# Kernel optimization log

Measured on AMD Instinct MI355X. Metric: run time of the kernel, lower is better.

## Reference

```python
import jax, jax.numpy as jnp
import numpy as np

H = 2048          # hidden_size
NH = 16           # num attention heads
NKV = 4           # num kv heads (GQA)
HD = 128          # head_dim (= v_head_dim)
E = 16            # n_routed_experts
K = 4             # num_experts_per_tok
DFF = 1024        # moe_intermediate_size
G = 4             # n_group
TG = 2            # topk_group
THETA = 1000000.0
EPS = 1e-6
B, S = 1, 1024


def _rmsnorm(x, w):
    return x * jax.lax.rsqrt(jnp.mean(x * x, axis=-1, keepdims=True) + EPS) * w


def _rope(pos, x):
    # neox-style rotary, full head_dim. x: [B,S,h,HD], pos: [B,S]
    half = HD // 2
    inv_freq = 1.0 / (THETA ** (jnp.arange(half, dtype=jnp.float32) / half))
    ang = pos[..., None].astype(jnp.float32) * inv_freq          # [B,S,half]
    cos = jnp.cos(ang)[:, :, None, :]
    sin = jnp.sin(ang)[:, :, None, :]
    x1, x2 = x[..., :half], x[..., half:]
    return jnp.concatenate([x1 * cos - x2 * sin, x2 * cos + x1 * sin], axis=-1)


def setup_inputs() -> dict:
    key = jax.random.key(0)
    ks = jax.random.split(key, 10)
    sc = 0.02
    return {
        "hidden_states": jax.random.normal(ks[0], (B, S, H), dtype=jnp.float32),
        "positions": jnp.arange(B * S, dtype=jnp.int64 if jax.config.jax_enable_x64 else jnp.int32).reshape(B, S),
        "in_norm_w": jnp.ones((H,), jnp.float32),
        "post_norm_w": jnp.ones((H,), jnp.float32),
        "qkv_w": jax.random.normal(ks[1], (H, (NH + 2 * NKV) * HD), jnp.float32) * sc,
        "o_w": jax.random.normal(ks[2], (NH * HD, H), jnp.float32) * sc,
        "gate_w": jax.random.normal(ks[3], (E, H), jnp.float32) * sc,
        "gate_bias": jax.random.normal(ks[4], (E,), jnp.float32) * sc,
        "gate_up_w": jax.random.normal(ks[5], (E, H, 2 * DFF), jnp.float32) * sc,
        "down_w": jax.random.normal(ks[6], (E, DFF, H), jnp.float32) * sc,
    }


def reference(hidden_states, positions, in_norm_w, post_norm_w, qkv_w, o_w,
              gate_w, gate_bias, gate_up_w, down_w):
    Bq, Sq, _ = hidden_states.shape
    T = Bq * Sq

    # ---- pre-norm attention ----
    residual = hidden_states
    h = _rmsnorm(hidden_states, in_norm_w)
    qkv = h @ qkv_w                                             # [B,S,(NH+2*NKV)*HD]
    q, k, v = jnp.split(qkv, [NH * HD, (NH + NKV) * HD], axis=-1)
    q = q.reshape(Bq, Sq, NH, HD)
    k = k.reshape(Bq, Sq, NKV, HD)
    v = v.reshape(Bq, Sq, NKV, HD)
    q = _rope(positions, q)
    k = _rope(positions, k)
    rep = NH // NKV
    k = jnp.repeat(k, rep, axis=2)                              # [B,S,NH,HD]
    v = jnp.repeat(v, rep, axis=2)
    scores = jnp.einsum('bqhd,bkhd->bhqk', q, k) * (HD ** -0.5)
    causal = jnp.tril(jnp.ones((Sq, Sq), bool))
    scores = jnp.where(causal, scores, -1e30)
    attn = jax.nn.softmax(scores, axis=-1)
    o = jnp.einsum('bhqk,bkhd->bqhd', attn, v).reshape(Bq, Sq, NH * HD)
    h = residual + o @ o_w

    # ---- pre-norm MoE ----
    residual = h
    x = _rmsnorm(h, post_norm_w).reshape(T, H)

    # gate (fp32), sigmoid scores + correction bias, grouped top-k (noaux_tc)
    logits = x.astype(jnp.float32) @ gate_w.T                   # [T,E]
    sig = jax.nn.sigmoid(logits)
    sb = sig + gate_bias.astype(jnp.float32)
    grp = sb.reshape(T, G, E // G)
    group_scores = jax.lax.top_k(grp, 2)[0].sum(-1)             # [T,G]
    _, gidx = jax.lax.top_k(group_scores, TG)
    gmask = jax.nn.one_hot(gidx, G, dtype=sb.dtype).sum(1)      # [T,G]
    emask = jnp.repeat(gmask, E // G, axis=1)                   # [T,E]
    masked = jnp.where(emask > 0, sb, -jnp.inf)
    _, tidx = jax.lax.top_k(masked, K)                          # [T,K]
    w = jnp.take_along_axis(sig, tidx, axis=1)
    w = w / (w.sum(-1, keepdims=True) + 1e-20)                  # renormalize

    # experts: dense compute, sparse combine
    gu = jnp.einsum('td,edf->etf', x, gate_up_w)                # [E,T,2*DFF]
    g, u = jnp.split(gu, 2, axis=-1)
    act = jax.nn.silu(g) * u
    y = jnp.einsum('etf,efd->etd', act, down_w)                 # [E,T,H]
    cw = jnp.zeros((T, E), jnp.float32).at[jnp.arange(T)[:, None], tidx].add(w)
    moe_out = jnp.einsum('te,etd->td', cw, y.astype(jnp.float32))
    return residual + moe_out.astype(hidden_states.dtype).reshape(Bq, Sq, H)
```

## Files before the change

kernel.cpp:

```cpp
#include <hip/hip_runtime.h>
#include <hip/hip_bf16.h>
#include <math.h>

#define H_DIM   2048
#define NH      16
#define NKV     4
#define HD      128
#define NE      16
#define TOPK    4
#define DFF     1024
#define NG      4
#define SEQ     1024
#define QKV_N   3072
#define EPS_RMS 1e-6f
#define THETA   1000000.0f

typedef __attribute__((ext_vector_type(8))) short bf16x8;
typedef __attribute__((ext_vector_type(4))) short s16x4;
typedef __attribute__((ext_vector_type(4))) float f32x4;

__device__ inline unsigned short f2bf(float x) {
    unsigned u = __builtin_bit_cast(unsigned, x);
    unsigned r = (u + 0x7FFFu + ((u >> 16) & 1u)) >> 16;
    return (unsigned short)r;
}

__device__ inline unsigned pk2bf(float lo, float hi) {
    __hip_bfloat162 h = __float22bfloat162_rn(float2{lo, hi});
    unsigned r;
    __builtin_memcpy(&r, &h, 4);
    return r;
}

__global__ __launch_bounds__(256) void w2bfT(const float* __restrict__ in,
                                             unsigned short* __restrict__ out,
                                             int K, int N) {
    const float* src = in + (size_t)blockIdx.z * K * N;
    unsigned short* dst = out + (size_t)blockIdx.z * K * N;
    int n0 = blockIdx.x * 64, k0 = blockIdx.y * 64;
    __shared__ unsigned short tile[64][66];
    int tid = threadIdx.x, c = tid & 63, r4 = tid >> 6;
    #pragma unroll
    for (int rep = 0; rep < 16; rep++) {
        int r = rep * 4 + r4;
        tile[r][c] = f2bf(src[(size_t)(k0 + r) * N + n0 + c]);
    }
    __syncthreads();
    #pragma unroll
    for (int rep = 0; rep < 16; rep++) {
        int r = rep * 4 + r4;
        dst[(size_t)(n0 + r) * K + k0 + c] = tile[c][r];
    }
}

__global__ __launch_bounds__(256) void rmsnorm_dual(const float* __restrict__ in,
                                                    const float* __restrict__ w,
                                                    float* __restrict__ outf,
                                                    unsigned short* __restrict__ outb) {
    int t = blockIdx.x;
    const float* xt = in + (size_t)t * H_DIM;
    float ss = 0.f;
    for (int d = threadIdx.x * 4; d < H_DIM; d += 1024) {
        float4 v = *reinterpret_cast<const float4*>(xt + d);
        ss += v.x * v.x + v.y * v.y + v.z * v.z + v.w * v.w;
    }
    for (int off = 1; off < 64; off <<= 1) ss += __shfl_xor(ss, off);
    __shared__ float red[4];
    __shared__ float srms;
    if ((threadIdx.x & 63) == 0) red[threadIdx.x >> 6] = ss;
    __syncthreads();
    if (threadIdx.x == 0)
        srms = rsqrtf((red[0] + red[1] + red[2] + red[3]) * (1.f / H_DIM) + EPS_RMS);
    __syncthreads();
    float r = srms;
    for (int d = threadIdx.x * 4; d < H_DIM; d += 1024) {
        float4 v  = *reinterpret_cast<const float4*>(xt + d);
        float4 wv = *reinterpret_cast<const float4*>(w + d);
        float4 ov;
        ov.x = v.x * r * wv.x; ov.y = v.y * r * wv.y;
        ov.z = v.z * r * wv.z; ov.w = v.w * r * wv.w;
        if (outf) *reinterpret_cast<float4*>(outf + (size_t)t * H_DIM + d) = ov;
        if (outb) {
            s16x4 bv = (s16x4){(short)f2bf(ov.x), (short)f2bf(ov.y),
                               (short)f2bf(ov.z), (short)f2bf(ov.w)};
            *reinterpret_cast<s16x4*>(outb + (size_t)t * H_DIM + d) = bv;
        }
    }
}

__global__ __launch_bounds__(128) void gemm_qkv_rope(const unsigned short* __restrict__ A,
                                                     const unsigned short* __restrict__ Bt,
                                                     const int* __restrict__ positions,
                                                     unsigned short* __restrict__ Qb,
                                                     unsigned short* __restrict__ Kb,
                                                     unsigned short* __restrict__ Vt) {
    __shared__ unsigned short As[8][66][8];
    __shared__ unsigned short Bs[8][130][8];
    int xb = blockIdx.x;
    int row0 = blockIdx.y * 64, col0 = xb * 128;
    int t = threadIdx.x;
    int w = t >> 6, lane = t & 63, lo = lane & 15, g = lane >> 4;
    int wr = w * 32;
    f32x4 acc[2][8];
    #pragma unroll
    for (int mi = 0; mi < 2; mi++)
        #pragma unroll
        for (int ni = 0; ni < 8; ni++) acc[mi][ni] = (f32x4){0.f, 0.f, 0.f, 0.f};
    int arow8 = t >> 3, ac = t & 7;
    size_t aoff[4], boff[8];
    #pragma unroll
    for (int rep = 0; rep < 4; rep++)
        aoff[rep] = (size_t)(row0 + rep * 16 + arow8) * H_DIM + ac * 8;
    #pragma unroll
    for (int rep = 0; rep < 8; rep++)
        boff[rep] = (size_t)(col0 + rep * 16 + arow8) * H_DIM + ac * 8;
    bf16x8 aR[4], bR[8];
    #pragma unroll
    for (int rep = 0; rep < 4; rep++) aR[rep] = *(const bf16x8*)(A + aoff[rep]);
    #pragma unroll
    for (int rep = 0; rep < 8; rep++) bR[rep] = *(const bf16x8*)(Bt + boff[rep]);
    for (int k0 = 0; k0 < H_DIM; k0 += 64) {
        #pragma unroll
        for (int rep = 0; rep < 4; rep++)
            *(bf16x8*)As[ac][rep * 16 + arow8] = aR[rep];
        #pragma unroll
        for (int rep = 0; rep < 8; rep++)
            *(bf16x8*)Bs[ac][rep * 16 + arow8] = bR[rep];
        int kn = k0 + 64;
        if (kn < H_DIM) {
            #pragma unroll
            for (int rep = 0; rep < 4; rep++) aR[rep] = *(const bf16x8*)(A + aoff[rep] + kn);
            #pragma unroll
            for (int rep = 0; rep < 8; rep++) bR[rep] = *(const bf16x8*)(Bt + boff[rep] + kn);
        }
        __syncthreads();
        #pragma unroll
        for (int kh = 0; kh < 2; kh++) {
            bf16x8 af[2], bfr[8];
            #pragma unroll
            for (int mi = 0; mi < 2; mi++) af[mi] = *(const bf16x8*)As[kh * 4 + g][wr + mi * 16 + lo];
            #pragma unroll
            for (int ni = 0; ni < 8; ni++) bfr[ni] = *(const bf16x8*)Bs[kh * 4 + g][ni * 16 + lo];
            #pragma unroll
            for (int mi = 0; mi < 2; mi++)
                #pragma unroll
                for (int ni = 0; ni < 8; ni++)
                    acc[mi][ni] = __builtin_amdgcn_mfma_f32_16x16x32_bf16(af[mi], bfr[ni], acc[mi][ni], 0, 0, 0);
        }
        __syncthreads();
    }
    if (xb < NH + NKV) {
        bool isQ = (xb < NH);
        unsigned short* dst = isQ ? (Qb + (size_t)xb * SEQ * HD)
                                  : (Kb + (size_t)(xb - NH) * SEQ * HD);
        float qs = isQ ? 0.08838834764831845f : 1.0f;
        float invf[4];
        #pragma unroll
        for (int ni = 0; ni < 4; ni++)
            invf[ni] = __powf(THETA, -(float)(ni * 16 + lo) * (1.0f / 64.0f));
        #pragma unroll
        for (int mi = 0; mi < 2; mi++)
            #pragma unroll
            for (int r = 0; r < 4; r++) {
                int tok = row0 + wr + mi * 16 + g * 4 + r;
                float pos = (float)positions[tok];
                #pragma unroll
                for (int ni = 0; ni < 4; ni++) {
                    float s, c;
                    __sincosf(pos * invf[ni], &s, &c);
                    float x1 = acc[mi][ni][r], x2 = acc[mi][ni + 4][r];
                    int d = ni * 16 + lo;
                    dst[(size_t)tok * HD + d]      = f2bf((x1 * c - x2 * s) * qs);
                    dst[(size_t)tok * HD + d + 64] = f2bf((x2 * c + x1 * s) * qs);
                }
            }
    } else {
        int kvh = xb - (NH + NKV);
        #pragma unroll
        for (int mi = 0; mi < 2; mi++)
            #pragma unroll
            for (int ni = 0; ni < 8; ni++) {
                int tok0 = row0 + wr + mi * 16 + g * 4;
                int d = ni * 16 + lo;
                ushort4 v4;
                v4.x = f2bf(acc[mi][ni][0]);
                v4.y = f2bf(acc[mi][ni][1]);
                v4.z = f2bf(acc[mi][ni][2]);
                v4.w = f2bf(acc[mi][ni][3]);
                *reinterpret_cast<ushort4*>(Vt + ((size_t)kvh * HD + d) * SEQ + tok0) = v4;
            }
    }
}

__global__ __launch_bounds__(256) void gemm_bf16(const unsigned short* __restrict__ A,
                                                 const unsigned short* __restrict__ Bt,
                                                 float* __restrict__ C,
                                                 float* __restrict__ C2,
                                                 const float* __restrict__ R,
                                                 int M, int N, int K) {
    __shared__ unsigned short As[8][130][8];
    __shared__ unsigned short Bs[8][66][8];
    int row0 = blockIdx.y * 128, col0 = blockIdx.x * 64;
    int t = threadIdx.x;
    int w = t >> 6, lane = t & 63, lo = lane & 15, g = lane >> 4;
    int wr = (w >> 1) * 64, wc = (w & 1) * 32;
    f32x4 acc[4][2];
    #pragma unroll
    for (int mi = 0; mi < 4; mi++)
        #pragma unroll
        for (int ni = 0; ni < 2; ni++) acc[mi][ni] = (f32x4){0.f, 0.f, 0.f, 0.f};
    int arow8 = t >> 3, ac = t & 7;
    size_t aoff[4], boff[2];
    #pragma unroll
    for (int rep = 0; rep < 4; rep++)
        aoff[rep] = (size_t)(row0 + rep * 32 + arow8) * K + ac * 8;
    #pragma unroll
    for (int rep = 0; rep < 2; rep++)
        boff[rep] = (size_t)(col0 + rep * 32 + arow8) * K + ac * 8;
    bf16x8 aR[4], bR[2];
    #pragma unroll
    for (int rep = 0; rep < 4; rep++) aR[rep] = *(const bf16x8*)(A + aoff[rep]);
    #pragma unroll
    for (int rep = 0; rep < 2; rep++) bR[rep] = *(const bf16x8*)(Bt + boff[rep]);
    for (int k0 = 0; k0 < K; k0 += 64) {
        #pragma unroll
        for (int rep = 0; rep < 4; rep++)
            *(bf16x8*)As[ac][rep * 32 + arow8] = aR[rep];
        #pragma unroll
        for (int rep = 0; rep < 2; rep++)
            *(bf16x8*)Bs[ac][rep * 32 + arow8] = bR[rep];
        int kn = k0 + 64;
        if (kn < K) {
            #pragma unroll
            for (int rep = 0; rep < 4; rep++) aR[rep] = *(const bf16x8*)(A + aoff[rep] + kn);
            #pragma unroll
            for (int rep = 0; rep < 2; rep++) bR[rep] = *(const bf16x8*)(Bt + boff[rep] + kn);
        }
        __syncthreads();
        #pragma unroll
        for (int kh = 0; kh < 2; kh++) {
            bf16x8 af[4], bfr[2];
            #pragma unroll
            for (int mi = 0; mi < 4; mi++) af[mi] = *(const bf16x8*)As[kh * 4 + g][wr + mi * 16 + lo];
            #pragma unroll
            for (int ni = 0; ni < 2; ni++) bfr[ni] = *(const bf16x8*)Bs[kh * 4 + g][wc + ni * 16 + lo];
            #pragma unroll
            for (int mi = 0; mi < 4; mi++)
                #pragma unroll
                for (int ni = 0; ni < 2; ni++)
                    acc[mi][ni] = __builtin_amdgcn_mfma_f32_16x16x32_bf16(af[mi], bfr[ni], acc[mi][ni], 0, 0, 0);
        }
        __syncthreads();
    }
    #pragma unroll
    for (int mi = 0; mi < 4; mi++)
        #pragma unroll
        for (int ni = 0; ni < 2; ni++)
            #pragma unroll
            for (int r = 0; r < 4; r++) {
                int row = row0 + wr + mi * 16 + g * 4 + r;
                int col = col0 + wc + ni * 16 + lo;
                size_t idx = (size_t)row * N + col;
                float v = acc[mi][ni][r];
                if (R)  v += R[idx];
                C[idx] = v;
                if (C2) C2[idx] = v;
            }
}

__global__ __launch_bounds__(256) void attn_mfma(const unsigned short* __restrict__ Qb,
                                                 const unsigned short* __restrict__ Kb,
                                                 const unsigned short* __restrict__ Vt,
                                                 unsigned short* __restrict__ ob) {
    int bx = blockIdx.x;
    int h  = blockIdx.y;
    int kvh = h >> 2;
    int tid = threadIdx.x;
    int wid = tid >> 6;
    int qsel = wid >> 1, khalf = wid & 1;
    int qt = qsel ? (SEQ / 16 - 1 - bx) : bx;
    int q0 = qt * 16;
    int l = tid & 63;
    int lo = l & 15, g = l >> 4;

    __shared__ alignas(16) unsigned short pbuf[4][16][40];
    __shared__ float obuf[2][16][128];
    __shared__ float mbuf[2][16], lbuf[2][16];

    bf16x8 qf[4];
    const unsigned short* qp = Qb + ((size_t)h * SEQ + q0 + lo) * HD + g * 8;
    #pragma unroll
    for (int ks = 0; ks < 4; ks++)
        qf[ks] = *(const bf16x8*)(qp + ks * 32);

    f32x4 accO[8];
    #pragma unroll
    for (int nd = 0; nd < 8; nd++) accO[nd] = (f32x4){0.f, 0.f, 0.f, 0.f};
    float mrun[4], lrun[4];
    #pragma unroll
    for (int r = 0; r < 4; r++) { mrun[r] = -INFINITY; lrun[r] = 0.f; }

    int nc = (q0 + 16 + 31) / 32;
    int ncH = (nc + 1) >> 1;
    int cbeg = khalf ? ncH : 0;
    int cend = khalf ? nc : ncH;
    for (int ch = cbeg; ch < cend; ch++) {
        int kv0 = ch * 32;
        f32x4 accS[2];
        accS[0] = (f32x4){0.f, 0.f, 0.f, 0.f};
        accS[1] = (f32x4){0.f, 0.f, 0.f, 0.f};
        const unsigned short* kp = Kb + ((size_t)kvh * SEQ + kv0 + lo) * HD + g * 8;
        #pragma unroll
        for (int n = 0; n < 2; n++) {
            const unsigned short* kpn = kp + (size_t)n * 16 * HD;
            #pragma unroll
            for (int ks = 0; ks < 4; ks++) {
                bf16x8 kf = *(const bf16x8*)(kpn + ks * 32);
                accS[n] = __builtin_amdgcn_mfma_f32_16x16x32_bf16(qf[ks], kf, accS[n], 0, 0, 0);
            }
        }
        if (ch == nc - 1) {
            #pragma unroll
            for (int n = 0; n < 2; n++)
                #pragma unroll
                for (int r = 0; r < 4; r++) {
                    int kv = kv0 + n * 16 + lo;
                    int q  = q0 + g * 4 + r;
                    if (kv > q) accS[n][r] = -1e30f;
                }
        }
        float mt[4], fac[4];
        #pragma unroll
        for (int r = 0; r < 4; r++) {
            float m = fmaxf(accS[0][r], accS[1][r]);
            #pragma unroll
            for (int off = 1; off < 16; off <<= 1) m = fmaxf(m, __shfl_xor(m, off));
            mt[r] = fmaxf(mrun[r], m);
            fac[r] = __expf(mrun[r] - mt[r]);
        }
        float psum[4] = {0.f, 0.f, 0.f, 0.f};
        #pragma unroll
        for (int n = 0; n < 2; n++)
            #pragma unroll
            for (int r = 0; r < 4; r++) {
                float p = __expf(accS[n][r] - mt[r]);
                psum[r] += p;
                pbuf[wid][g * 4 + r][n * 16 + lo] = f2bf(p);
            }
        #pragma unroll
        for (int r = 0; r < 4; r++) {
            float s = psum[r];
            #pragma unroll
            for (int off = 1; off < 16; off <<= 1) s += __shfl_xor(s, off);
            lrun[r] = lrun[r] * fac[r] + s;
            mrun[r] = mt[r];
        }
        #pragma unroll
        for (int nd = 0; nd < 8; nd++)
            #pragma unroll
            for (int r = 0; r < 4; r++) accO[nd][r] *= fac[r];
        __builtin_amdgcn_sched_barrier(0);
        bf16x8 pf = *(const bf16x8*)(&pbuf[wid][lo][g * 8]);
        const unsigned short* vp = Vt + ((size_t)kvh * HD + lo) * SEQ + kv0 + g * 8;
        #pragma unroll
        for (int nd = 0; nd < 8; nd++) {
            bf16x8 vf = *(const bf16x8*)(vp + (size_t)nd * 16 * SEQ);
            accO[nd] = __builtin_amdgcn_mfma_f32_16x16x32_bf16(pf, vf, accO[nd], 0, 0, 0);
        }
        __builtin_amdgcn_sched_barrier(0);
    }
    if (khalf) {
        #pragma unroll
        for (int r = 0; r < 4; r++) {
            if (lo == 0) {
                mbuf[qsel][g * 4 + r] = mrun[r];
                lbuf[qsel][g * 4 + r] = lrun[r];
            }
            #pragma unroll
            for (int nd = 0; nd < 8; nd++)
                obuf[qsel][g * 4 + r][nd * 16 + lo] = accO[nd][r];
        }
    }
    __syncthreads();
    if (!khalf) {
        #pragma unroll
        for (int r = 0; r < 4; r++) {
            int row = g * 4 + r;
            float m1 = mbuf[qsel][row], l1 = lbuf[qsel][row];
            float m0 = mrun[r], l0 = lrun[r];
            float m = fmaxf(m0, m1);
            float f0 = (l0 > 0.f) ? __expf(m0 - m) : 0.f;
            float f1 = (l1 > 0.f) ? __expf(m1 - m) : 0.f;
            float linv = 1.f / (l0 * f0 + l1 * f1);
            #pragma unroll
            for (int nd = 0; nd < 8; nd++) {
                float v = (accO[nd][r] * f0 + obuf[qsel][row][nd * 16 + lo] * f1) * linv;
                ob[(size_t)(q0 + row) * H_DIM + h * HD + nd * 16 + lo] = f2bf(v);
            }
        }
    }
}

__global__ __launch_bounds__(256) void router_kernel(const float* __restrict__ x,
                                                     const float* __restrict__ gate_w,
                                                     const float* __restrict__ gate_bias,
                                                     int* __restrict__ toklist,
                                                     float* __restrict__ tokw,
                                                     int* __restrict__ cnt) {
    int t = blockIdx.x;
    const float* xt = x + (size_t)t * H_DIM;
    __shared__ float logits[NE];
    int wid = threadIdx.x >> 6, lane = threadIdx.x & 63;
    #pragma unroll
    for (int i = 0; i < 4; i++) {
        int e = wid * 4 + i;
        const float* gw = gate_w + (size_t)e * H_DIM;
        float p = 0.f;
        for (int d = lane * 4; d < H_DIM; d += 256) {
            float4 xv = *reinterpret_cast<const float4*>(xt + d);
            float4 wv = *reinterpret_cast<const float4*>(gw + d);
            p += xv.x * wv.x + xv.y * wv.y + xv.z * wv.z + xv.w * wv.w;
        }
        #pragma unroll
        for (int off = 1; off < 64; off <<= 1) p += __shfl_xor(p, off);
        if (lane == 0) logits[e] = p;
    }
    __syncthreads();
    if (threadIdx.x == 0) {
        float sig[NE], sb[NE];
        for (int e = 0; e < NE; e++) {
            sig[e] = 1.f / (1.f + expf(-logits[e]));
            sb[e] = sig[e] + gate_bias[e];
        }
        float gs[NG];
        for (int g = 0; g < NG; g++) {
            float m1 = -1e30f, m2 = -1e30f;
            for (int i = 0; i < 4; i++) {
                float v = sb[g * 4 + i];
                if (v > m1) { m2 = m1; m1 = v; } else if (v > m2) m2 = v;
            }
            gs[g] = m1 + m2;
        }
        int g1 = 0;
        for (int g = 1; g < NG; g++) if (gs[g] > gs[g1]) g1 = g;
        int g2 = -1;
        for (int g = 0; g < NG; g++) {
            if (g == g1) continue;
            if (g2 < 0 || gs[g] > gs[g2]) g2 = g;
        }
        bool allowed[NE], used[NE];
        for (int e = 0; e < NE; e++) { int g = e >> 2; allowed[e] = (g == g1 || g == g2); used[e] = false; }
        int sel[TOPK]; float wsel[TOPK]; float wsum = 0.f;
        for (int k = 0; k < TOPK; k++) {
            int best = -1; float bv = -1e30f;
            for (int e = 0; e < NE; e++) {
                if (!allowed[e] || used[e]) continue;
                if (best < 0 || sb[e] > bv) { best = e; bv = sb[e]; }
            }
            used[best] = true; sel[k] = best; wsel[k] = sig[best]; wsum += sig[best];
        }
        float invs = 1.f / (wsum + 1e-20f);
        for (int k = 0; k < TOPK; k++) {
            int e = sel[k];
            int slot = atomicAdd(&cnt[e], 1);
            toklist[e * SEQ + slot] = t;
            tokw[e * SEQ + slot] = wsel[k] * invs;
        }
    }
}

__global__ void prefix_kernel(const int* __restrict__ cnt, int* __restrict__ base) {
    if (threadIdx.x == 0) {
        int s = 0;
        for (int e = 0; e < NE; e++) { base[e] = s; s += cnt[e]; }
    }
}

__global__ __launch_bounds__(256, 2) void moe_gemm1_mfma(const unsigned short* __restrict__ xb,
                                                         const float* __restrict__ gup,
                                                         const int* __restrict__ toklist,
                                                         const int* __restrict__ cnt,
                                                         const int* __restrict__ base,
                                                         unsigned short* __restrict__ act) {
    int e = blockIdx.z;
    int ce = cnt[e];
    int t0 = blockIdx.y * 256;
    if (t0 >= ce) return;
    int f0 = blockIdx.x * 32;
    __shared__ unsigned short As[8][258][8];
    __shared__ unsigned short BsG[8][33][8];
    __shared__ unsigned short BsU[8][33][8];
    __shared__ int toks[256];
    int t = threadIdx.x;
    { int s = t0 + t; toks[t] = toklist[e * SEQ + (s < ce ? s : 0)]; }
    __syncthreads();
    int w = t >> 6, lane = t & 63, lo = lane & 15, g = lane >> 4;
    int wrb = w * 64;
    f32x4 accG[4][2], accU[4][2];
    #pragma unroll
    for (int mi = 0; mi < 4; mi++)
        #pragma unroll
        for (int ni = 0; ni < 2; ni++) {
            accG[mi][ni] = (f32x4){0.f, 0.f, 0.f, 0.f};
            accU[mi][ni] = (f32x4){0.f, 0.f, 0.f, 0.f};
        }
    int arow8 = t >> 3, ac = t & 7;
    size_t abase[8];
    #pragma unroll
    for (int rep = 0; rep < 8; rep++)
        abase[rep] = (size_t)toks[rep * 32 + arow8] * H_DIM + ac * 8;
    int half = t >> 7, tt = t & 127;
    int rp = tt >> 3, nq = tt & 7;
    int kgB = rp >> 2, wq = (rp & 3) * 2;
    unsigned short (*Bsel)[33][8] = half ? BsU : BsG;
    const float* W = gup + (size_t)e * H_DIM * (2 * DFF);
    const float* pB0 = W + (size_t)(2 * rp) * (2 * DFF) + half * DFF + f0 + nq * 4;
    bf16x8 aR[8];
    #pragma unroll
    for (int rep = 0; rep < 8; rep++) aR[rep] = *(const bf16x8*)(xb + abase[rep]);
    f32x4 bR0 = *(const f32x4*)pB0;
    f32x4 bR1 = *(const f32x4*)(pB0 + 2 * DFF);
    f32x4 bR2 = *(const f32x4*)(pB0 + (size_t)32 * 2 * DFF);
    f32x4 bR3 = *(const f32x4*)(pB0 + (size_t)33 * 2 * DFF);
    for (int k0 = 0; k0 < H_DIM; k0 += 64) {
        #pragma unroll
        for (int rep = 0; rep < 8; rep++)
            *(bf16x8*)As[ac][rep * 32 + arow8] = aR[rep];
        #pragma unroll
        for (int j = 0; j < 4; j++) {
            *(unsigned*)&Bsel[kgB][nq * 4 + j][wq]     = pk2bf(bR0[j], bR1[j]);
            *(unsigned*)&Bsel[kgB + 4][nq * 4 + j][wq] = pk2bf(bR2[j], bR3[j]);
        }
        int kn = k0 + 64;
        if (kn < H_DIM) {
            #pragma unroll
            for (int rep = 0; rep < 8; rep++)
                aR[rep] = *(const bf16x8*)(xb + abase[rep] + kn);
            const float* pB = pB0 + (size_t)kn * (2 * DFF);
            bR0 = *(const f32x4*)pB;
            bR1 = *(const f32x4*)(pB + 2 * DFF);
            bR2 = *(const f32x4*)(pB + (size_t)32 * 2 * DFF);
            bR3 = *(const f32x4*)(pB + (size_t)33 * 2 * DFF);
        }
        __syncthreads();
        #pragma unroll
        for (int kh = 0; kh < 2; kh++) {
            bf16x8 af[4], bg[2], bu[2];
            #pragma unroll
            for (int mi = 0; mi < 4; mi++) af[mi] = *(const bf16x8*)As[kh * 4 + g][wrb + mi * 16 + lo];
            #pragma unroll
            for (int ni = 0; ni < 2; ni++) {
                bg[ni] = *(const bf16x8*)BsG[kh * 4 + g][ni * 16 + lo];
                bu[ni] = *(const bf16x8*)BsU[kh * 4 + g][ni * 16 + lo];
            }
            #pragma unroll
            for (int mi = 0; mi < 4; mi++)
                #pragma unroll
                for (int ni = 0; ni < 2; ni++) {
                    accG[mi][ni] = __builtin_amdgcn_mfma_f32_16x16x32_bf16(af[mi], bg[ni], accG[mi][ni], 0, 0, 0);
                    accU[mi][ni] = __builtin_amdgcn_mfma_f32_16x16x32_bf16(af[mi], bu[ni], accU[mi][ni], 0, 0, 0);
                }
        }
        __syncthreads();
    }
    int b = base[e];
    #pragma unroll
    for (int mi = 0; mi < 4; mi++)
        #pragma unroll
        for (int ni = 0; ni < 2; ni++)
            #pragma unroll
            for (int r = 0; r < 4; r++) {
                int slot = t0 + wrb + mi * 16 + g * 4 + r;
                if (slot < ce) {
                    float gv = accG[mi][ni][r], uv = accU[mi][ni][r];
                    float a = (gv / (1.f + __expf(-gv))) * uv;
                    act[(size_t)(b + slot) * DFF + f0 + ni * 16 + lo] = f2bf(a);
                }
            }
}

__global__ __launch_bounds__(256, 4) void moe_gemm2_mfma(const unsigned short* __restrict__ act,
                                                         const float* __restrict__ down,
                                                         const int* __restrict__ toklist,
                                                         const float* __restrict__ tokw,
                                                         const int* __restrict__ cnt,
                                                         const int* __restrict__ base,
                                                         float* __restrict__ out) {
    int e = blockIdx.z;
    int ce = cnt[e];
    int t0 = blockIdx.y * 256;
    if (t0 >= ce) return;
    int c0 = blockIdx.x * 32;
    __shared__ unsigned short As[8][258][8];
    __shared__ unsigned short Bs[8][33][8];
    int t = threadIdx.x;
    int w = t >> 6, lane = t & 63, lo = lane & 15, g = lane >> 4;
    int wrb = w * 64;
    int b = base[e];
    f32x4 acc[4][2];
    #pragma unroll
    for (int mi = 0; mi < 4; mi++)
        #pragma unroll
        for (int ni = 0; ni < 2; ni++) acc[mi][ni] = (f32x4){0.f, 0.f, 0.f, 0.f};
    int arow8 = t >> 3, ac = t & 7;
    size_t abase[8];
    #pragma unroll
    for (int rep = 0; rep < 8; rep++) {
        int slot = t0 + rep * 32 + arow8;
        abase[rep] = (size_t)(b + (slot < ce ? slot : t0)) * DFF + ac * 8;
    }
    int tt = t & 127;
    int rp = tt >> 3, nq = tt & 7;
    int kgB = rp >> 2, wq = (rp & 3) * 2;
    const float* pB0 = down + (size_t)e * DFF * H_DIM + (size_t)(2 * rp) * H_DIM + c0 + nq * 4;
    bool stageB = (t < 128);
    bf16x8 aR[8];
    #pragma unroll
    for (int rep = 0; rep < 8; rep++) aR[rep] = *(const bf16x8*)(act + abase[rep]);
    f32x4 bR0 = (f32x4){0.f,0.f,0.f,0.f}, bR1 = bR0, bR2 = bR0, bR3 = bR0;
    if (stageB) {
        bR0 = *(const f32x4*)pB0;
        bR1 = *(const f32x4*)(pB0 + H_DIM);
        bR2 = *(const f32x4*)(pB0 + (size_t)32 * H_DIM);
        bR3 = *(const f32x4*)(pB0 + (size_t)33 * H_DIM);
    }
    for (int k0 = 0; k0 < DFF; k0 += 64) {
        #pragma unroll
        for (int rep = 0; rep < 8; rep++)
            *(bf16x8*)As[ac][rep * 32 + arow8] = aR[rep];
        if (stageB) {
            #pragma unroll
            for (int j = 0; j < 4; j++) {
                *(unsigned*)&Bs[kgB][nq * 4 + j][wq]     = pk2bf(bR0[j], bR1[j]);
                *(unsigned*)&Bs[kgB + 4][nq * 4 + j][wq] = pk2bf(bR2[j], bR3[j]);
            }
        }
        int kn = k0 + 64;
        if (kn < DFF) {
            #pragma unroll
            for (int rep = 0; rep < 8; rep++)
                aR[rep] = *(const bf16x8*)(act + abase[rep] + kn);
            if (stageB) {
                const float* pB = pB0 + (size_t)kn * H_DIM;
                bR0 = *(const f32x4*)pB;
                bR1 = *(const f32x4*)(pB + H_DIM);
                bR2 = *(const f32x4*)(pB + (size_t)32 * H_DIM);
                bR3 = *(const f32x4*)(pB + (size_t)33 * H_DIM);
            }
        }
        __syncthreads();
        #pragma unroll
        for (int kh = 0; kh < 2; kh++) {
            bf16x8 af[4], bfr[2];
            #pragma unroll
            for (int mi = 0; mi < 4; mi++) af[mi] = *(const bf16x8*)As[kh * 4 + g][wrb + mi * 16 + lo];
            #pragma unroll
            for (int ni = 0; ni < 2; ni++) bfr[ni] = *(const bf16x8*)Bs[kh * 4 + g][ni * 16 + lo];
            #pragma unroll
            for (int mi = 0; mi < 4; mi++)
                #pragma unroll
                for (int ni = 0; ni < 2; ni++)
                    acc[mi][ni] = __builtin_amdgcn_mfma_f32_16x16x32_bf16(af[mi], bfr[ni], acc[mi][ni], 0, 0, 0);
        }
        __syncthreads();
    }
    #pragma unroll
    for (int mi = 0; mi < 4; mi++)
        #pragma unroll
        for (int r = 0; r < 4; r++) {
            int slot = t0 + wrb + mi * 16 + g * 4 + r;
            if (slot < ce) {
                int tok = toklist[e * SEQ + slot];
                float wt = tokw[e * SEQ + slot];
                #pragma unroll
                for (int ni = 0; ni < 2; ni++)
                    atomicAdd(&out[(size_t)tok * H_DIM + c0 + ni * 16 + lo],
                              wt * acc[mi][ni][r]);
            }
        }
}

extern "C" void kernel_launch(void* const* d_in, const int* in_sizes, int n_in,
                              void* d_out, int out_size, void* d_ws, size_t ws_size,
                              hipStream_t stream) {
    const float* hidden     = (const float*)d_in[0];
    const int*   positions  = (const int*)d_in[1];
    const float* in_norm_w  = (const float*)d_in[2];
    const float* post_norm_w= (const float*)d_in[3];
    const float* qkv_w      = (const float*)d_in[4];
    const float* o_w        = (const float*)d_in[5];
    const float* gate_w     = (const float*)d_in[6];
    const float* gate_bias  = (const float*)d_in[7];
    const float* gate_up_w  = (const float*)d_in[8];
    const float* down_w     = (const float*)d_in[9];
    float* out = (float*)d_out;

    float* ws   = (float*)d_ws;
    float* h2   = ws;
    float* x    = h2  + (size_t)SEQ * H_DIM;
    float* tokw = x   + (size_t)SEQ * H_DIM;
    int* toklist = (int*)(tokw + NE * SEQ);
    int* cnt  = toklist + NE * SEQ;
    int* base = cnt + NE;
    unsigned short* hb = (unsigned short*)(base + NE);
    unsigned short* ob = hb + (size_t)SEQ * H_DIM;
    unsigned short* xbuf = ob + (size_t)SEQ * H_DIM;
    unsigned short* act = xbuf + (size_t)SEQ * H_DIM;
    unsigned short* Qb = act + (size_t)4 * SEQ * DFF;
    unsigned short* Kb = Qb + (size_t)NH * SEQ * HD;
    unsigned short* Vt = Kb + (size_t)NKV * SEQ * HD;
    unsigned short* qkvT = Vt + (size_t)NKV * HD * SEQ;
    unsigned short* oT   = qkvT + (size_t)QKV_N * H_DIM;

    w2bfT<<<dim3(QKV_N / 64, H_DIM / 64, 1), 256, 0, stream>>>(qkv_w, qkvT, H_DIM, QKV_N);
    w2bfT<<<dim3(H_DIM / 64, H_DIM / 64, 1), 256, 0, stream>>>(o_w, oT, H_DIM, H_DIM);

    rmsnorm_dual<<<SEQ, 256, 0, stream>>>(hidden, in_norm_w, nullptr, hb);
    gemm_qkv_rope<<<dim3(QKV_N / 128, SEQ / 64), 128, 0, stream>>>(hb, qkvT, positions, Qb, Kb, Vt);
    attn_mfma<<<dim3(SEQ / 32, NH), 256, 0, stream>>>(Qb, Kb, Vt, ob);
    gemm_bf16<<<dim3(H_DIM / 64, SEQ / 128), 256, 0, stream>>>(ob, oT, h2, out, hidden,
                                                               SEQ, H_DIM, H_DIM);
    rmsnorm_dual<<<SEQ, 256, 0, stream>>>(h2, post_norm_w, x, xbuf);
    (void)hipMemsetAsync(cnt, 0, NE * sizeof(int), stream);
    router_kernel<<<SEQ, 256, 0, stream>>>(x, gate_w, gate_bias, toklist, tokw, cnt);
    prefix_kernel<<<1, 64, 0, stream>>>(cnt, base);
    moe_gemm1_mfma<<<dim3(DFF / 32, SEQ / 256, NE), 256, 0, stream>>>(xbuf, gate_up_w, toklist, cnt, base, act);
    moe_gemm2_mfma<<<dim3(H_DIM / 32, SEQ / 256, NE), 256, 0, stream>>>(act, down_w, toklist, tokw, cnt, base, out);
}
```

Before: 382.5 us.

## Double-buffer LDS tiles in MoE gate-up GEMM to drop one barrier per step

Converts the shared-memory A/B tiles of moe_gemm1 into ping-pong buffers, so the next tile is written to the alternate buffer while MFMAs consume the current one. This leaves one __syncthreads per k-step instead of two. It also removes the padding rows (258->256, 33->32), which may bring back LDS bank conflicts, and drops the shared toks staging in favour of direct global index loads. Doubling the LDS footprint may lower occupancy.

```diff
diff --git a/kernel.cpp b/kernel.cpp
--- a/kernel.cpp
+++ b/kernel.cpp
@@ -487,13 +487,10 @@
     int t0 = blockIdx.y * 256;
     if (t0 >= ce) return;
     int f0 = blockIdx.x * 32;
-    __shared__ unsigned short As[8][258][8];
-    __shared__ unsigned short BsG[8][33][8];
-    __shared__ unsigned short BsU[8][33][8];
-    __shared__ int toks[256];
+    __shared__ unsigned short As[2][8][256][8];
+    __shared__ unsigned short BsG[2][8][32][8];
+    __shared__ unsigned short BsU[2][8][32][8];
     int t = threadIdx.x;
-    { int s = t0 + t; toks[t] = toklist[e * SEQ + (s < ce ? s : 0)]; }
-    __syncthreads();
     int w = t >> 6, lane = t & 63, lo = lane & 15, g = lane >> 4;
     int wrb = w * 64;
     f32x4 accG[4][2], accU[4][2];
@@ -507,51 +504,48 @@
     int arow8 = t >> 3, ac = t & 7;
     size_t abase[8];
     #pragma unroll
-    for (int rep = 0; rep < 8; rep++)
-        abase[rep] = (size_t)toks[rep * 32 + arow8] * H_DIM + ac * 8;
+    for (int rep = 0; rep < 8; rep++) {
+        int s = t0 + rep * 32 + arow8;
+        int idx = (s < ce) ? s : 0;
+        abase[rep] = (size_t)toklist[e * SEQ + idx] * H_DIM + ac * 8;
+    }
     int half = t >> 7, tt = t & 127;
     int rp = tt >> 3, nq = tt & 7;
     int kgB = rp >> 2, wq = (rp & 3) * 2;
-    unsigned short (*Bsel)[33][8] = half ? BsU : BsG;
+    unsigned short (*BselBuf)[8][32][8] = half ? BsU : BsG;
     const float* W = gup + (size_t)e * H_DIM * (2 * DFF);
     const float* pB0 = W + (size_t)(2 * rp) * (2 * DFF) + half * DFF + f0 + nq * 4;
+
+#define M1_LOAD(kk) { _Pragma("unroll") \
+    for (int rep = 0; rep < 8; rep++) aR[rep] = *(const bf16x8*)(xb + abase[rep] + (kk)); \
+    const float* pB = pB0 + (size_t)(kk) * (2 * DFF); \
+    bR0 = *(const f32x4*)pB; bR1 = *(const f32x4*)(pB + 2 * DFF); \
+    bR2 = *(const f32x4*)(pB + (size_t)32 * 2 * DFF); bR3 = *(const f32x4*)(pB + (size_t)33 * 2 * DFF); }
+#define M1_STAGE(d) { _Pragma("unroll") \
+    for (int rep = 0; rep < 8; rep++) *(bf16x8*)As[d][ac][rep * 32 + arow8] = aR[rep]; \
+    _Pragma("unroll") for (int j = 0; j < 4; j++) { \
+        *(unsigned*)&BselBuf[d][kgB][nq * 4 + j][wq]     = pk2bf(bR0[j], bR1[j]); \
+        *(unsigned*)&BselBuf[d][kgB + 4][nq * 4 + j][wq] = pk2bf(bR2[j], bR3[j]); } }
+
     bf16x8 aR[8];
-    #pragma unroll
-    for (int rep = 0; rep < 8; rep++) aR[rep] = *(const bf16x8*)(xb + abase[rep]);
-    f32x4 bR0 = *(const f32x4*)pB0;
-    f32x4 bR1 = *(const f32x4*)(pB0 + 2 * DFF);
-    f32x4 bR2 = *(const f32x4*)(pB0 + (size_t)32 * 2 * DFF);
-    f32x4 bR3 = *(const f32x4*)(pB0 + (size_t)33 * 2 * DFF);
+    f32x4 bR0, bR1, bR2, bR3;
+    M1_LOAD(0);
+    M1_STAGE(0);
+    M1_LOAD(64);
+    __syncthreads();
+    int cur = 0;
     for (int k0 = 0; k0 < H_DIM; k0 += 64) {
-        #pragma unroll
-        for (int rep = 0; rep < 8; rep++)
-            *(bf16x8*)As[ac][rep * 32 + arow8] = aR[rep];
-        #pragma unroll
-        for (int j = 0; j < 4; j++) {
-            *(unsigned*)&Bsel[kgB][nq * 4 + j][wq]     = pk2bf(bR0[j], bR1[j]);
-            *(unsigned*)&Bsel[kgB + 4][nq * 4 + j][wq] = pk2bf(bR2[j], bR3[j]);
-        }
         int kn = k0 + 64;
-        if (kn < H_DIM) {
-            #pragma unroll
-            for (int rep = 0; rep < 8; rep++)
-                aR[rep] = *(const bf16x8*)(xb + abase[rep] + kn);
-            const float* pB = pB0 + (size_t)kn * (2 * DFF);
-            bR0 = *(const f32x4*)pB;
-            bR1 = *(const f32x4*)(pB + 2 * DFF);
-            bR2 = *(const f32x4*)(pB + (size_t)32 * 2 * DFF);
-            bR3 = *(const f32x4*)(pB + (size_t)33 * 2 * DFF);
-        }
-        __syncthreads();
+        if (kn < H_DIM) M1_STAGE(cur ^ 1);
         #pragma unroll
         for (int kh = 0; kh < 2; kh++) {
             bf16x8 af[4], bg[2], bu[2];
             #pragma unroll
-            for (int mi = 0; mi < 4; mi++) af[mi] = *(const bf16x8*)As[kh * 4 + g][wrb + mi * 16 + lo];
+            for (int mi = 0; mi < 4; mi++) af[mi] = *(const bf16x8*)As[cur][kh * 4 + g][wrb + mi * 16 + lo];
             #pragma unroll
             for (int ni = 0; ni < 2; ni++) {
-                bg[ni] = *(const bf16x8*)BsG[kh * 4 + g][ni * 16 + lo];
-                bu[ni] = *(const bf16x8*)BsU[kh * 4 + g][ni * 16 + lo];
+                bg[ni] = *(const bf16x8*)BsG[cur][kh * 4 + g][ni * 16 + lo];
+                bu[ni] = *(const bf16x8*)BsU[cur][kh * 4 + g][ni * 16 + lo];
             }
             #pragma unroll
             for (int mi = 0; mi < 4; mi++)
@@ -561,7 +555,10 @@
                     accU[mi][ni] = __builtin_amdgcn_mfma_f32_16x16x32_bf16(af[mi], bu[ni], accU[mi][ni], 0, 0, 0);
                 }
         }
+        int kf = k0 + 128;
+        if (kf < H_DIM) M1_LOAD(kf);
         __syncthreads();
+        cur ^= 1;
     }
     int b = base[e];
     #pragma unroll
```

New measurement: 434.2 us. 1.14x slower.

## Split MoE gate-up GEMM over K into two halves with separate SiLU combine

Applied to the files above, without the earlier changes.

The first MoE GEMM now splits the hidden-dim reduction into two halves, doubling the grid so more blocks run concurrently. Each half writes fp32 partial gate and up sums to workspace planes. A new elementwise kernel then adds the halves, applies SiLU-mul and writes bf16 activations. This trades extra global traffic (about 64MB of fp32 partials written and read back) and one more launch for more parallelism in a grid that is sparse because many expert tiles exit early.

```diff
diff --git a/kernel.cpp b/kernel.cpp
--- a/kernel.cpp
+++ b/kernel.cpp
@@ -481,12 +481,17 @@
                                                          const int* __restrict__ toklist,
                                                          const int* __restrict__ cnt,
                                                          const int* __restrict__ base,
-                                                         unsigned short* __restrict__ act) {
+                                                         float* __restrict__ pG,
+                                                         float* __restrict__ pU) {
     int e = blockIdx.z;
     int ce = cnt[e];
-    int t0 = blockIdx.y * 256;
+    int yb = blockIdx.y;
+    int khalf = yb & 1;
+    int t0 = (yb >> 1) * 256;
     if (t0 >= ce) return;
     int f0 = blockIdx.x * 32;
+    const int KB = H_DIM / 2;
+    int kbeg = khalf * KB;
     __shared__ unsigned short As[8][258][8];
     __shared__ unsigned short BsG[8][33][8];
     __shared__ unsigned short BsU[8][33][8];
@@ -517,12 +522,13 @@
     const float* pB0 = W + (size_t)(2 * rp) * (2 * DFF) + half * DFF + f0 + nq * 4;
     bf16x8 aR[8];
     #pragma unroll
-    for (int rep = 0; rep < 8; rep++) aR[rep] = *(const bf16x8*)(xb + abase[rep]);
-    f32x4 bR0 = *(const f32x4*)pB0;
-    f32x4 bR1 = *(const f32x4*)(pB0 + 2 * DFF);
-    f32x4 bR2 = *(const f32x4*)(pB0 + (size_t)32 * 2 * DFF);
-    f32x4 bR3 = *(const f32x4*)(pB0 + (size_t)33 * 2 * DFF);
-    for (int k0 = 0; k0 < H_DIM; k0 += 64) {
+    for (int rep = 0; rep < 8; rep++) aR[rep] = *(const bf16x8*)(xb + abase[rep] + kbeg);
+    const float* pBb = pB0 + (size_t)kbeg * (2 * DFF);
+    f32x4 bR0 = *(const f32x4*)pBb;
+    f32x4 bR1 = *(const f32x4*)(pBb + 2 * DFF);
+    f32x4 bR2 = *(const f32x4*)(pBb + (size_t)32 * 2 * DFF);
+    f32x4 bR3 = *(const f32x4*)(pBb + (size_t)33 * 2 * DFF);
+    for (int k0 = kbeg; k0 < kbeg + KB; k0 += 64) {
         #pragma unroll
         for (int rep = 0; rep < 8; rep++)
             *(bf16x8*)As[ac][rep * 32 + arow8] = aR[rep];
@@ -532,7 +538,7 @@
             *(unsigned*)&Bsel[kgB + 4][nq * 4 + j][wq] = pk2bf(bR2[j], bR3[j]);
         }
         int kn = k0 + 64;
-        if (kn < H_DIM) {
+        if (kn < kbeg + KB) {
             #pragma unroll
             for (int rep = 0; rep < 8; rep++)
                 aR[rep] = *(const bf16x8*)(xb + abase[rep] + kn);
@@ -564,6 +570,7 @@
         __syncthreads();
     }
     int b = base[e];
+    size_t plane = (size_t)khalf * 4096 * DFF;
     #pragma unroll
     for (int mi = 0; mi < 4; mi++)
         #pragma unroll
@@ -572,11 +579,42 @@
             for (int r = 0; r < 4; r++) {
                 int slot = t0 + wrb + mi * 16 + g * 4 + r;
                 if (slot < ce) {
-                    float gv = accG[mi][ni][r], uv = accU[mi][ni][r];
-                    float a = (gv / (1.f + __expf(-gv))) * uv;
-                    act[(size_t)(b + slot) * DFF + f0 + ni * 16 + lo] = f2bf(a);
+                    size_t idx = plane + (size_t)(b + slot) * DFF + f0 + ni * 16 + lo;
+                    pG[idx] = accG[mi][ni][r];
+                    pU[idx] = accU[mi][ni][r];
                 }
             }
+}
+
+__global__ __launch_bounds__(256) void moe_silu_combine(const float* __restrict__ pG,
+                                                        const float* __restrict__ pU,
+                                                        unsigned short* __restrict__ act) {
+    size_t i = ((size_t)blockIdx.x * 256 + threadIdx.x) * 8;
+    const size_t plane = (size_t)4096 * DFF;
+    f32x4 g0 = *(const f32x4*)(pG + i);
+    f32x4 g1 = *(const f32x4*)(pG + plane + i);
+    f32x4 g2 = *(const f32x4*)(pG + i + 4);
+    f32x4 g3 = *(const f32x4*)(pG + plane + i + 4);
+    f32x4 u0 = *(const f32x4*)(pU + i);
+    f32x4 u1 = *(const f32x4*)(pU + plane + i);
+    f32x4 u2 = *(const f32x4*)(pU + i + 4);
+    f32x4 u3 = *(const f32x4*)(pU + plane + i + 4);
+    bf16x8 o;
+    #pragma unroll
+    for (int j = 0; j < 4; j++) {
+        float gv = g0[j] + g1[j];
+        float uv = u0[j] + u1[j];
+        float a = (gv / (1.f + __expf(-gv))) * uv;
+        o[j] = (short)f2bf(a);
+    }
+    #pragma unroll
+    for (int j = 0; j < 4; j++) {
+        float gv = g2[j] + g3[j];
+        float uv = u2[j] + u3[j];
+        float a = (gv / (1.f + __expf(-gv))) * uv;
+        o[4 + j] = (short)f2bf(a);
+    }
+    *(bf16x8*)(act + i) = o;
 }
 
 __global__ __launch_bounds__(256, 4) void moe_gemm2_mfma(const unsigned short* __restrict__ act,
@@ -711,6 +749,8 @@
     unsigned short* Vt = Kb + (size_t)NKV * SEQ * HD;
     unsigned short* qkvT = Vt + (size_t)NKV * HD * SEQ;
     unsigned short* oT   = qkvT + (size_t)QKV_N * H_DIM;
+    float* pG = (float*)(oT + (size_t)H_DIM * H_DIM);
+    float* pU = pG + (size_t)2 * 4096 * DFF;
 
     w2bfT<<<dim3(QKV_N / 64, H_DIM / 64, 1), 256, 0, stream>>>(qkv_w, qkvT, H_DIM, QKV_N);
     w2bfT<<<dim3(H_DIM / 64, H_DIM / 64, 1), 256, 0, stream>>>(o_w, oT, H_DIM, H_DIM);
@@ -724,6 +764,8 @@
     (void)hipMemsetAsync(cnt, 0, NE * sizeof(int), stream);
     router_kernel<<<SEQ, 256, 0, stream>>>(x, gate_w, gate_bias, toklist, tokw, cnt);
     prefix_kernel<<<1, 64, 0, stream>>>(cnt, base);
-    moe_gemm1_mfma<<<dim3(DFF / 32, SEQ / 256, NE), 256, 0, stream>>>(xbuf, gate_up_w, toklist, cnt, base, act);
+    moe_gemm1_mfma<<<dim3(DFF / 32, (SEQ / 256) * 2, NE), 256, 0, stream>>>(xbuf, gate_up_w, toklist,
+                                                                            cnt, base, pG, pU);
+    moe_silu_combine<<<(4096 * DFF) / (256 * 8), 256, 0, stream>>>(pG, pU, act);
     moe_gemm2_mfma<<<dim3(H_DIM / 32, SEQ / 256, NE), 256, 0, stream>>>(act, down_w, toklist, tokw, cnt, base, out);
 }
```

Result: slower. 397.3 us (+3.9%).

## Fuse o_proj weight conversion into GEMM and inline expert prefix sums

Applied to the files above, without the earlier changes.

The o_proj GEMM now reads the fp32 weight directly in its natural [K,N] layout and converts it to bf16 while staging it into shared memory. This removes the separate transpose/convert kernel and its 16 MB round trip. Separately, the one-thread prefix kernel is dropped and each MoE GEMM block sums the preceding expert counts itself. In exchange, the GEMM does the fp32 loads and conversions per tile, reading twice the bytes for B and packing scattered values into LDS.

```diff
diff --git a/kernel.cpp b/kernel.cpp
--- a/kernel.cpp
+++ b/kernel.cpp
@@ -192,12 +192,12 @@
     }
 }
 
-__global__ __launch_bounds__(256) void gemm_bf16(const unsigned short* __restrict__ A,
-                                                 const unsigned short* __restrict__ Bt,
-                                                 float* __restrict__ C,
-                                                 float* __restrict__ C2,
-                                                 const float* __restrict__ R,
-                                                 int M, int N, int K) {
+__global__ __launch_bounds__(256) void gemm_oproj(const unsigned short* __restrict__ A,
+                                                  const float* __restrict__ B,
+                                                  float* __restrict__ C,
+                                                  float* __restrict__ C2,
+                                                  const float* __restrict__ R,
+                                                  int M, int N, int K) {
     __shared__ unsigned short As[8][130][8];
     __shared__ unsigned short Bs[8][66][8];
     int row0 = blockIdx.y * 128, col0 = blockIdx.x * 64;
@@ -210,31 +210,38 @@
         #pragma unroll
         for (int ni = 0; ni < 2; ni++) acc[mi][ni] = (f32x4){0.f, 0.f, 0.f, 0.f};
     int arow8 = t >> 3, ac = t & 7;
-    size_t aoff[4], boff[2];
+    size_t aoff[4];
     #pragma unroll
     for (int rep = 0; rep < 4; rep++)
         aoff[rep] = (size_t)(row0 + rep * 32 + arow8) * K + ac * 8;
-    #pragma unroll
-    for (int rep = 0; rep < 2; rep++)
-        boff[rep] = (size_t)(col0 + rep * 32 + arow8) * K + ac * 8;
-    bf16x8 aR[4], bR[2];
+    int rp = t >> 4, nq = t & 15;
+    int kgB = rp >> 2, wq = (rp & 3) * 2;
+    const float* pB0 = B + (size_t)(2 * rp) * N + col0 + nq * 4;
+    bf16x8 aR[4];
     #pragma unroll
     for (int rep = 0; rep < 4; rep++) aR[rep] = *(const bf16x8*)(A + aoff[rep]);
-    #pragma unroll
-    for (int rep = 0; rep < 2; rep++) bR[rep] = *(const bf16x8*)(Bt + boff[rep]);
+    f32x4 bR0 = *(const f32x4*)pB0;
+    f32x4 bR1 = *(const f32x4*)(pB0 + N);
+    f32x4 bR2 = *(const f32x4*)(pB0 + (size_t)32 * N);
+    f32x4 bR3 = *(const f32x4*)(pB0 + (size_t)33 * N);
     for (int k0 = 0; k0 < K; k0 += 64) {
         #pragma unroll
         for (int rep = 0; rep < 4; rep++)
             *(bf16x8*)As[ac][rep * 32 + arow8] = aR[rep];
         #pragma unroll
-        for (int rep = 0; rep < 2; rep++)
-            *(bf16x8*)Bs[ac][rep * 32 + arow8] = bR[rep];
+        for (int j = 0; j < 4; j++) {
+            *(unsigned*)&Bs[kgB][nq * 4 + j][wq]     = pk2bf(bR0[j], bR1[j]);
+            *(unsigned*)&Bs[kgB + 4][nq * 4 + j][wq] = pk2bf(bR2[j], bR3[j]);
+        }
         int kn = k0 + 64;
         if (kn < K) {
             #pragma unroll
             for (int rep = 0; rep < 4; rep++) aR[rep] = *(const bf16x8*)(A + aoff[rep] + kn);
-            #pragma unroll
-            for (int rep = 0; rep < 2; rep++) bR[rep] = *(const bf16x8*)(Bt + boff[rep] + kn);
+            const float* pB = pB0 + (size_t)kn * N;
+            bR0 = *(const f32x4*)pB;
+            bR1 = *(const f32x4*)(pB + N);
+            bR2 = *(const f32x4*)(pB + (size_t)32 * N);
+            bR3 = *(const f32x4*)(pB + (size_t)33 * N);
         }
         __syncthreads();
         #pragma unroll
@@ -469,18 +476,10 @@
     }
 }
 
-__global__ void prefix_kernel(const int* __restrict__ cnt, int* __restrict__ base) {
-    if (threadIdx.x == 0) {
-        int s = 0;
-        for (int e = 0; e < NE; e++) { base[e] = s; s += cnt[e]; }
-    }
-}
-
 __global__ __launch_bounds__(256, 2) void moe_gemm1_mfma(const unsigned short* __restrict__ xb,
                                                          const float* __restrict__ gup,
                                                          const int* __restrict__ toklist,
                                                          const int* __restrict__ cnt,
-                                                         const int* __restrict__ base,
                                                          unsigned short* __restrict__ act) {
     int e = blockIdx.z;
     int ce = cnt[e];
@@ -563,7 +562,8 @@
         }
         __syncthreads();
     }
-    int b = base[e];
+    int b = 0;
+    for (int ee = 0; ee < e; ee++) b += cnt[ee];
     #pragma unroll
     for (int mi = 0; mi < 4; mi++)
         #pragma unroll
@@ -584,7 +584,6 @@
                                                          const int* __restrict__ toklist,
                                                          const float* __restrict__ tokw,
                                                          const int* __restrict__ cnt,
-                                                         const int* __restrict__ base,
                                                          float* __restrict__ out) {
     int e = blockIdx.z;
     int ce = cnt[e];
@@ -596,7 +595,8 @@
     int t = threadIdx.x;
     int w = t >> 6, lane = t & 63, lo = lane & 15, g = lane >> 4;
     int wrb = w * 64;
-    int b = base[e];
+    int b = 0;
+    for (int ee = 0; ee < e; ee++) b += cnt[ee];
     f32x4 acc[4][2];
     #pragma unroll
     for (int mi = 0; mi < 4; mi++)
@@ -710,20 +710,17 @@
     unsigned short* Kb = Qb + (size_t)NH * SEQ * HD;
     unsigned short* Vt = Kb + (size_t)NKV * SEQ * HD;
     unsigned short* qkvT = Vt + (size_t)NKV * HD * SEQ;
-    unsigned short* oT   = qkvT + (size_t)QKV_N * H_DIM;
 
     w2bfT<<<dim3(QKV_N / 64, H_DIM / 64, 1), 256, 0, stream>>>(qkv_w, qkvT, H_DIM, QKV_N);
-    w2bfT<<<dim3(H_DIM / 64, H_DIM / 64, 1), 256, 0, stream>>>(o_w, oT, H_DIM, H_DIM);
 
     rmsnorm_dual<<<SEQ, 256, 0, stream>>>(hidden, in_norm_w, nullptr, hb);
     gemm_qkv_rope<<<dim3(QKV_N / 128, SEQ / 64), 128, 0, stream>>>(hb, qkvT, positions, Qb, Kb, Vt);
     attn_mfma<<<dim3(SEQ / 32, NH), 256, 0, stream>>>(Qb, Kb, Vt, ob);
-    gemm_bf16<<<dim3(H_DIM / 64, SEQ / 128), 256, 0, stream>>>(ob, oT, h2, out, hidden,
-                                                               SEQ, H_DIM, H_DIM);
+    gemm_oproj<<<dim3(H_DIM / 64, SEQ / 128), 256, 0, stream>>>(ob, o_w, h2, out, hidden,
+                                                                SEQ, H_DIM, H_DIM);
     rmsnorm_dual<<<SEQ, 256, 0, stream>>>(h2, post_norm_w, x, xbuf);
     (void)hipMemsetAsync(cnt, 0, NE * sizeof(int), stream);
     router_kernel<<<SEQ, 256, 0, stream>>>(x, gate_w, gate_bias, toklist, tokw, cnt);
-    prefix_kernel<<<1, 64, 0, stream>>>(cnt, base);
-    moe_gemm1_mfma<<<dim3(DFF / 32, SEQ / 256, NE), 256, 0, stream>>>(xbuf, gate_up_w, toklist, cnt, base, act);
-    moe_gemm2_mfma<<<dim3(H_DIM / 32, SEQ / 256, NE), 256, 0, stream>>>(act, down_w, toklist, tokw, cnt, base, out);
-}
+    moe_gemm1_mfma<<<dim3(DFF / 32, SEQ / 256, NE), 256, 0, stream>>>(xbuf, gate_up_w, toklist, cnt, act);
+    moe_gemm2_mfma<<<dim3(H_DIM / 32, SEQ / 256, NE), 256, 0, stream>>>(act, down_w, toklist, tokw, cnt, out);
+}
```

After: 380.3 us (median of 3 runs). Within noise of the previous version (-0.6%).
